# Optimization experiments

Measured on AMD Instinct MI355X. Metric: run time of the kernel, lower is better.

The kernel has to match this reference:

```python
import jax, jax.numpy as jnp
import numpy as np

H = 8        # n_heads (== n_kv_heads)
D = 128      # head_dim
WINDOW = 16  # sliding window (left); causal => right window = 0
EPS = 1e-6   # qk_norm_eps


def rms_norm(x, w, eps=EPS):
    # RMSNorm over last dim with learnable scale
    ms = jnp.mean(jnp.square(x), axis=-1, keepdims=True)
    return x * jax.lax.rsqrt(ms + eps) * w


def setup_inputs() -> dict:
    key = jax.random.key(0)
    ks = jax.random.split(key, 5)
    B, S, dim = 4, 2048, 1024
    scale = 1.0 / np.sqrt(dim)
    return {
        "x": jax.random.normal(ks[0], (B, S, dim), jnp.float32),
        "wq": jax.random.normal(ks[1], (dim, dim), jnp.float32) * scale,
        "wk": jax.random.normal(ks[2], (dim, dim), jnp.float32) * scale,
        "wv": jax.random.normal(ks[3], (dim, dim), jnp.float32) * scale,
        "wo": jax.random.normal(ks[4], (dim, dim), jnp.float32) * scale,
        "q_norm_w": jnp.ones((dim,), jnp.float32),
        "k_norm_w": jnp.ones((dim,), jnp.float32),
    }


def reference(x, wq, wk, wv, wo, q_norm_w, k_norm_w):
    B, S, dim = x.shape
    # projections (torch Linear: x @ W.T)
    xq = rms_norm(x @ wq.T, q_norm_w)
    xk = rms_norm(x @ wk.T, k_norm_w)
    xv = x @ wv.T
    q = xq.reshape(B, S, H, D)
    k = xk.reshape(B, S, H, D)
    v = xv.reshape(B, S, H, D)

    # ALiBi slopes for 8 heads (power of two): 2^-1 .. 2^-8
    slopes = jnp.exp2(-jnp.arange(1, H + 1, dtype=jnp.float32))
    pos = jnp.arange(S)
    rel = pos[None, :] - pos[:, None]          # [S, S], rel[i, j] = j - i
    bias = slopes[:, None, None] * rel.astype(x.dtype)   # [H, S, S]
    masked = (rel > 0) | (rel < -WINDOW)       # causal + sliding window
    bias = jnp.where(masked[None], -jnp.inf, bias)

    scores = jnp.einsum('bqhd,bkhd->bhqk', q, k) / np.sqrt(D) + bias[None]
    attn = jax.nn.softmax(scores, axis=-1)
    out = jnp.einsum('bhqk,bkhd->bqhd', attn, v).reshape(B, S, H * D)
    return out @ wo.T
```

## Files before the change

### kernel.cpp

```cpp
#include <hip/hip_runtime.h>
#include <math.h>

#define NHEADS 8
#define HDIM   128
#define WIN    16
#define DIM    1024
#define QKVDIM 3072
#define SEQ    2048
#define BATCH  4
#define MROWS  (BATCH * SEQ)
#define RMS_EPS 1e-6f

typedef __bf16 bf16x8 __attribute__((ext_vector_type(8)));
typedef unsigned short u16x8 __attribute__((ext_vector_type(8)));
typedef float  f32x4  __attribute__((ext_vector_type(4)));

__device__ __forceinline__ unsigned short f2b(float f) {
    union { float f; unsigned u; } c; c.f = f;
    return (unsigned short)((c.u + 0x7FFFu + ((c.u >> 16) & 1u)) >> 16);
}
__device__ __forceinline__ float b2f(unsigned short u) {
    union { unsigned u; float f; } c; c.u = ((unsigned)u) << 16; return c.f;
}
__device__ __forceinline__ bf16x8 u2b(u16x8 u) {
    union { u16x8 u; bf16x8 b; } c; c.u = u; return c.b;
}

__device__ __forceinline__ void storec(unsigned short* p, float v) { *p = f2b(v); }
__device__ __forceinline__ void storec(float* p, float v) { *p = v; }

__global__ __launch_bounds__(256) void cast_all(const float* __restrict__ x,
                                                const float* __restrict__ w0,
                                                const float* __restrict__ w1,
                                                const float* __restrict__ w2,
                                                const float* __restrict__ w3,
                                                unsigned short* __restrict__ xb,
                                                unsigned short* __restrict__ wb,
                                                float* __restrict__ sumsq)
{
    const int b = blockIdx.x;
    const int t = threadIdx.x;
    if (b >= 12288) {
        ((float4*)sumsq)[(b - 12288) * 256 + t] = make_float4(0.f, 0.f, 0.f, 0.f);
        return;
    }
    const float* src;
    unsigned short* dst;
    int i;
    if (b < 8192) {
        i = b * 256 + t;
        src = x; dst = xb;
    } else {
        const int bb = b - 8192;
        const int which = bb >> 10;
        i = (bb & 1023) * 256 + t;
        src = which == 0 ? w0 : which == 1 ? w1 : which == 2 ? w2 : w3;
        dst = wb + (size_t)which * DIM * DIM;
    }
    const float4 v = ((const float4*)src)[i];
    ushort4 o;
    o.x = f2b(v.x); o.y = f2b(v.y); o.z = f2b(v.z); o.w = f2b(v.w);
    ((ushort4*)dst)[i] = o;
}

template <typename TC>
__global__ __launch_bounds__(256) void gemm_nt_mfma(const unsigned short* __restrict__ A,
                                                    const unsigned short* __restrict__ B,
                                                    TC* __restrict__ C,
                                                    float* __restrict__ sumsq,
                                                    int M, int N, int K)
{
    __shared__ __align__(16) __bf16 As[128 * 64];
    __shared__ __align__(16) __bf16 Bs[128 * 64];

    const int t    = threadIdx.x;
    const int w    = t >> 6;
    const int lane = t & 63;
    const int wm   = w >> 1;
    const int wn   = w & 1;
    const int bm0  = blockIdx.y * 128;
    const int bn0  = blockIdx.x * 128;

    const int lrow   = lane >> 3;
    const int lchunk = (lane & 7) ^ (lrow & 7);
    const size_t laneoff = (size_t)lrow * K + lchunk * 8;

    const unsigned short* gA = A + (size_t)bm0 * K + laneoff;
    const unsigned short* gB = B + (size_t)bn0 * K + laneoff;

    const int frow = lane & 15;
    const int quad = lane >> 4;
    const int cs0 = ((quad    ) ^ (frow & 7)) * 8;
    const int cs1 = ((quad + 4) ^ (frow & 7)) * 8;

    f32x4 acc[4][4];
    #pragma unroll
    for (int i = 0; i < 4; ++i)
        #pragma unroll
        for (int j = 0; j < 4; ++j)
            #pragma unroll
            for (int e = 0; e < 4; ++e) acc[i][j][e] = 0.f;

    for (int kt = 0; kt < K; kt += 64) {
        __syncthreads();
        #pragma unroll
        for (int s = 0; s < 4; ++s) {
            const int seg = w * 4 + s;
            __builtin_amdgcn_global_load_lds(
                (const __attribute__((address_space(1))) void*)(gA + (size_t)seg * 8 * K + kt),
                (__attribute__((address_space(3))) void*)&As[seg * 512], 16, 0, 0);
            __builtin_amdgcn_global_load_lds(
                (const __attribute__((address_space(1))) void*)(gB + (size_t)seg * 8 * K + kt),
                (__attribute__((address_space(3))) void*)&Bs[seg * 512], 16, 0, 0);
        }
        __syncthreads();

        #pragma unroll
        for (int sub = 0; sub < 2; ++sub) {
            const int cs = sub ? cs1 : cs0;
            bf16x8 af[4], bg[4];
            #pragma unroll
            for (int i = 0; i < 4; ++i) {
                af[i] = *(const bf16x8*)&As[(wm * 64 + i * 16 + frow) * 64 + cs];
                bg[i] = *(const bf16x8*)&Bs[(wn * 64 + i * 16 + frow) * 64 + cs];
            }
            #pragma unroll
            for (int i = 0; i < 4; ++i)
                #pragma unroll
                for (int j = 0; j < 4; ++j)
                    acc[i][j] = __builtin_amdgcn_mfma_f32_16x16x32_bf16(af[i], bg[j], acc[i][j], 0, 0, 0);
        }
    }

    const int m_base = bm0 + wm * 64;
    const int n_base = bn0 + wn * 64;
    const int col    = frow;
    const int rquad  = quad * 4;
    #pragma unroll
    for (int i = 0; i < 4; ++i)
        #pragma unroll
        for (int r = 0; r < 4; ++r) {
            TC* crow = C + (size_t)(m_base + i * 16 + rquad + r) * N + n_base + col;
            #pragma unroll
            for (int j = 0; j < 4; ++j)
                storec(crow + j * 16, acc[i][j][r]);
        }

    if (sumsq != nullptr && bn0 < 2 * DIM) {
        const int which = bn0 >> 10;
        #pragma unroll
        for (int i = 0; i < 4; ++i)
            #pragma unroll
            for (int r = 0; r < 4; ++r) {
                float p = acc[i][0][r] * acc[i][0][r] + acc[i][1][r] * acc[i][1][r]
                        + acc[i][2][r] * acc[i][2][r] + acc[i][3][r] * acc[i][3][r];
                p += __shfl_xor(p, 1, 64);
                p += __shfl_xor(p, 2, 64);
                p += __shfl_xor(p, 4, 64);
                p += __shfl_xor(p, 8, 64);
                if (frow == 0)
                    atomicAdd(&sumsq[(size_t)(m_base + i * 16 + rquad + r) * 2 + which], p);
            }
    }
}

__global__ __launch_bounds__(256) void attn_mfma(const unsigned short* __restrict__ qkv,
                                                 const float* __restrict__ sumsq,
                                                 const float* __restrict__ qw,
                                                 const float* __restrict__ kw,
                                                 unsigned short* __restrict__ o)
{
    __shared__ __align__(16) unsigned short Klds[80 * 136];
    __shared__ __align__(16) unsigned short Vt[128 * 88];
    __shared__ __align__(16) unsigned short Plds[4 * 16 * 40];

    const int t  = threadIdx.x;
    const int qb = blockIdx.x;
    const int h  = blockIdx.y;
    const int r0 = qb * 64;
    const int i0 = r0 & (SEQ - 1);
    const int bb = r0 - i0;

    const unsigned short* kg = qkv + DIM + h * HDIM;
    const unsigned short* vg = qkv + 2 * DIM + h * HDIM;

    #pragma unroll
    for (int it = 0; it < 5; ++it) {
        const int c = it * 256 + t;
        {
            const int lr = c >> 4, c8 = c & 15;
            const int ks = i0 - 16 + lr;
            const int rc = ks < 0 ? 0 : ks;
            const float ksc = rsqrtf(sumsq[(size_t)(bb + rc) * 2 + 1] * (1.0f / DIM) + RMS_EPS);
            const u16x8 kv = *(const u16x8*)(kg + (size_t)(bb + rc) * QKVDIM + c8 * 8);
            u16x8 ko;
            #pragma unroll
            for (int e = 0; e < 8; ++e)
                ko[e] = f2b(b2f(kv[e]) * ksc * kw[h * HDIM + c8 * 8 + e]);
            *(u16x8*)&Klds[lr * 136 + c8 * 8] = ko;
        }
        {
            const int c8 = c / 80, lr = c - c8 * 80;
            const int ks = i0 - 16 + lr;
            const int rc = ks < 0 ? 0 : ks;
            const u16x8 vv = *(const u16x8*)(vg + (size_t)(bb + rc) * QKVDIM + c8 * 8);
            #pragma unroll
            for (int e = 0; e < 8; ++e)
                Vt[(c8 * 8 + e) * 88 + lr] = vv[e];
        }
    }
    __syncthreads();

    const int w    = t >> 6;
    const int lane = t & 63;
    const int frow = lane & 15;
    const int quad = lane >> 4;
    const int fk   = quad * 8;

    f32x4 s0 = {0.f, 0.f, 0.f, 0.f}, s1 = {0.f, 0.f, 0.f, 0.f};
    const unsigned short* qg = qkv + h * HDIM;
    const size_t qrow = (size_t)(r0 + w * 16 + frow) * QKVDIM;
    const float qsc = rsqrtf(sumsq[(size_t)(r0 + w * 16 + frow) * 2] * (1.0f / DIM) + RMS_EPS);
    #pragma unroll
    for (int kt = 0; kt < 4; ++kt) {
        const u16x8 qa = *(const u16x8*)(qg + qrow + kt * 32 + fk);
        u16x8 qn;
        #pragma unroll
        for (int e = 0; e < 8; ++e)
            qn[e] = f2b(b2f(qa[e]) * qsc * qw[h * HDIM + kt * 32 + fk + e]);
        const bf16x8 af = u2b(qn);
        const bf16x8 b0 = *(const bf16x8*)&Klds[(w * 16 + frow) * 136 + kt * 32 + fk];
        const bf16x8 b1 = *(const bf16x8*)&Klds[(w * 16 + 16 + frow) * 136 + kt * 32 + fk];
        s0 = __builtin_amdgcn_mfma_f32_16x16x32_bf16(af, b0, s0, 0, 0, 0);
        s1 = __builtin_amdgcn_mfma_f32_16x16x32_bf16(af, b1, s1, 0, 0, 0);
    }

    const float scl   = 0.088388347648318447f;
    const float slope = exp2f(-(float)(h + 1));
    const bool  lead  = (i0 == 0) && (w == 0);
    const int   col   = frow;
    float inv[4];
    #pragma unroll
    for (int r = 0; r < 4; ++r) {
        const int m = quad * 4 + r;
        float v0 = (col < m || lead) ? -1e30f : s0[r] * scl + slope * (float)(col - 16 - m);
        float v1 = (col > m)         ? -1e30f : s1[r] * scl + slope * (float)(col - m);
        float mx = fmaxf(v0, v1);
        #pragma unroll
        for (int off = 1; off < 16; off <<= 1) mx = fmaxf(mx, __shfl_xor(mx, off, 64));
        const float e0 = __expf(v0 - mx);
        const float e1 = __expf(v1 - mx);
        float sm = e0 + e1;
        #pragma unroll
        for (int off = 1; off < 16; off <<= 1) sm += __shfl_xor(sm, off, 64);
        inv[r] = 1.0f / sm;
        Plds[(w * 16 + m) * 40 + col]      = f2b(e0);
        Plds[(w * 16 + m) * 40 + 16 + col] = f2b(e1);
    }

    const bf16x8 pf = *(const bf16x8*)&Plds[(w * 16 + frow) * 40 + fk];
    f32x4 oa[8];
    #pragma unroll
    for (int nt = 0; nt < 8; ++nt) {
        oa[nt][0] = 0.f; oa[nt][1] = 0.f; oa[nt][2] = 0.f; oa[nt][3] = 0.f;
        const bf16x8 vf = *(const bf16x8*)&Vt[(nt * 16 + frow) * 88 + w * 16 + fk];
        oa[nt] = __builtin_amdgcn_mfma_f32_16x16x32_bf16(pf, vf, oa[nt], 0, 0, 0);
    }

    #pragma unroll
    for (int nt = 0; nt < 8; ++nt)
        #pragma unroll
        for (int r = 0; r < 4; ++r) {
            const int m = quad * 4 + r;
            o[(size_t)(r0 + w * 16 + m) * DIM + h * HDIM + nt * 16 + col] =
                f2b(oa[nt][r] * inv[r]);
        }
}

extern "C" void kernel_launch(void* const* d_in, const int* in_sizes, int n_in,
                              void* d_out, int out_size, void* d_ws, size_t ws_size,
                              hipStream_t stream)
{
    const float* x  = (const float*)d_in[0];
    const float* wq = (const float*)d_in[1];
    const float* wk = (const float*)d_in[2];
    const float* wv = (const float*)d_in[3];
    const float* wo = (const float*)d_in[4];
    const float* qw = (const float*)d_in[5];
    const float* kw = (const float*)d_in[6];
    float* out = (float*)d_out;

    unsigned short* xb   = (unsigned short*)d_ws;
    unsigned short* wb   = xb + (size_t)MROWS * DIM;
    unsigned short* xqkv = wb + (size_t)4 * DIM * DIM;
    unsigned short* ob   = xqkv + (size_t)MROWS * QKVDIM;
    float*          ssq  = (float*)(ob + (size_t)MROWS * DIM);
    unsigned short* wob  = wb + (size_t)3 * DIM * DIM;

    cast_all<<<12304, 256, 0, stream>>>(x, wq, wk, wv, wo, xb, wb, ssq);

    gemm_nt_mfma<unsigned short><<<dim3(QKVDIM / 128, MROWS / 128), 256, 0, stream>>>(
        xb, wb, xqkv, ssq, MROWS, QKVDIM, DIM);

    attn_mfma<<<dim3(MROWS / 64, NHEADS), 256, 0, stream>>>(xqkv, ssq, qw, kw, ob);

    gemm_nt_mfma<float><<<dim3(DIM / 128, MROWS / 128), 256, 0, stream>>>(
        ob, wob, out, nullptr, MROWS, DIM, DIM);
}
```

Before: 222.2 us.

## Replace GEMM with 256x256-tile double-buffered ping-pong MFMA kernel

Rewrites the projection GEMM to use 256x256 block tiles with 512 threads (8 waves, 2x4 wave grid), double-buffered LDS and global_load_lds prefetching interleaved with MFMA clusters separated by explicit barriers and vmcnt waits. s_setprio raises priority around MFMA bursts. The aim is to hide global-load latency and raise arithmetic intensity per LDS byte. In exchange it uses 128KB of LDS per block and many more accumulator registers. The larger tiles also give fewer blocks (e.g. 128 for the output GEMM), which may underfill the 256 CUs.

```diff
diff --git a/kernel.cpp b/kernel.cpp
--- a/kernel.cpp
+++ b/kernel.cpp
@@ -63,103 +63,150 @@
     ((ushort4*)dst)[i] = o;
 }
 
+#define BARR do { asm volatile("s_barrier" ::: "memory"); __builtin_amdgcn_sched_barrier(0); } while (0)
+#define WAITV(N) asm volatile("s_waitcnt vmcnt(" #N ")" ::: "memory")
+
+#define LDA8(mh, b) { \
+    _Pragma("unroll") for (int il = 0; il < 4; ++il) { \
+        const int rr = (wm * 128 + (mh) * 64 + il * 16 + frow) * 64; \
+        af[il][0] = *(const bf16x8*)&As[b][rr + cs0]; \
+        af[il][1] = *(const bf16x8*)&As[b][rr + cs1]; \
+    } }
+
+#define LDB4(nh, b, bgr) { \
+    _Pragma("unroll") for (int jl = 0; jl < 2; ++jl) { \
+        const int rr = (wn * 64 + (nh) * 32 + jl * 16 + frow) * 64; \
+        bgr[jl][0] = *(const bf16x8*)&Bs[b][rr + cs0]; \
+        bgr[jl][1] = *(const bf16x8*)&Bs[b][rr + cs1]; \
+    } }
+
+#define MMA16(mh, nh, bgr) { \
+    __builtin_amdgcn_s_setprio(1); \
+    _Pragma("unroll") for (int il = 0; il < 4; ++il) \
+    _Pragma("unroll") for (int jl = 0; jl < 2; ++jl) { \
+        acc[(mh)*4+il][(nh)*2+jl] = __builtin_amdgcn_mfma_f32_16x16x32_bf16(af[il][0], bgr[jl][0], acc[(mh)*4+il][(nh)*2+jl], 0, 0, 0); \
+        acc[(mh)*4+il][(nh)*2+jl] = __builtin_amdgcn_mfma_f32_16x16x32_bf16(af[il][1], bgr[jl][1], acc[(mh)*4+il][(nh)*2+jl], 0, 0, 0); \
+    } \
+    __builtin_amdgcn_s_setprio(0); }
+
+#define STAGE_A(b, half, kt) { \
+    _Pragma("unroll") for (int s2 = 0; s2 < 2; ++s2) { \
+        const int rb = (half) * 128 + s2 * 64; \
+        __builtin_amdgcn_global_load_lds( \
+            (const __attribute__((address_space(1))) void*)(gA + (size_t)rb * K + (kt)), \
+            (__attribute__((address_space(3))) void*)&As[b][(rb + wid * 8) * 64], 16, 0, 0); \
+    } }
+
+#define STAGE_B(b, half, kt) { \
+    _Pragma("unroll") for (int s2 = 0; s2 < 2; ++s2) { \
+        const int rb = (half) * 128 + s2 * 64; \
+        __builtin_amdgcn_global_load_lds( \
+            (const __attribute__((address_space(1))) void*)(gB + (size_t)rb * K + (kt)), \
+            (__attribute__((address_space(3))) void*)&Bs[b][(rb + wid * 8) * 64], 16, 0, 0); \
+    } }
+
 template <typename TC>
-__global__ __launch_bounds__(256) void gemm_nt_mfma(const unsigned short* __restrict__ A,
-                                                    const unsigned short* __restrict__ B,
-                                                    TC* __restrict__ C,
-                                                    float* __restrict__ sumsq,
-                                                    int M, int N, int K)
+__global__ __launch_bounds__(512, 2) void gemm_nt_256(const unsigned short* __restrict__ A,
+                                                      const unsigned short* __restrict__ B,
+                                                      TC* __restrict__ C,
+                                                      float* __restrict__ sumsq,
+                                                      int M, int N, int K)
 {
-    __shared__ __align__(16) __bf16 As[128 * 64];
-    __shared__ __align__(16) __bf16 Bs[128 * 64];
+    __shared__ __align__(16) __bf16 As[2][256 * 64];
+    __shared__ __align__(16) __bf16 Bs[2][256 * 64];
 
     const int t    = threadIdx.x;
-    const int w    = t >> 6;
+    const int wid  = t >> 6;
     const int lane = t & 63;
-    const int wm   = w >> 1;
-    const int wn   = w & 1;
-    const int bm0  = blockIdx.y * 128;
-    const int bn0  = blockIdx.x * 128;
-
-    const int lrow   = lane >> 3;
-    const int lchunk = (lane & 7) ^ (lrow & 7);
-    const size_t laneoff = (size_t)lrow * K + lchunk * 8;
-
-    const unsigned short* gA = A + (size_t)bm0 * K + laneoff;
-    const unsigned short* gB = B + (size_t)bn0 * K + laneoff;
+    const int wm   = wid >> 2;
+    const int wn   = wid & 3;
+    const int bm0  = blockIdx.y * 256;
+    const int bn0  = blockIdx.x * 256;
 
     const int frow = lane & 15;
     const int quad = lane >> 4;
-    const int cs0 = ((quad    ) ^ (frow & 7)) * 8;
-    const int cs1 = ((quad + 4) ^ (frow & 7)) * 8;
-
-    f32x4 acc[4][4];
-    #pragma unroll
-    for (int i = 0; i < 4; ++i)
+    const int cs0  = ((quad    ) ^ (frow & 7)) * 8;
+    const int cs1  = ((quad + 4) ^ (frow & 7)) * 8;
+
+    const int lr = lane >> 3;
+    const int lc = (lane & 7) ^ lr;
+    const unsigned short* gA = A + (size_t)(bm0 + wid * 8 + lr) * K + lc * 8;
+    const unsigned short* gB = B + (size_t)(bn0 + wid * 8 + lr) * K + lc * 8;
+
+    f32x4 acc[8][4];
+    #pragma unroll
+    for (int i = 0; i < 8; ++i)
         #pragma unroll
         for (int j = 0; j < 4; ++j)
             #pragma unroll
             for (int e = 0; e < 4; ++e) acc[i][j][e] = 0.f;
 
-    for (int kt = 0; kt < K; kt += 64) {
-        __syncthreads();
-        #pragma unroll
-        for (int s = 0; s < 4; ++s) {
-            const int seg = w * 4 + s;
-            __builtin_amdgcn_global_load_lds(
-                (const __attribute__((address_space(1))) void*)(gA + (size_t)seg * 8 * K + kt),
-                (__attribute__((address_space(3))) void*)&As[seg * 512], 16, 0, 0);
-            __builtin_amdgcn_global_load_lds(
-                (const __attribute__((address_space(1))) void*)(gB + (size_t)seg * 8 * K + kt),
-                (__attribute__((address_space(3))) void*)&Bs[seg * 512], 16, 0, 0);
-        }
-        __syncthreads();
-
-        #pragma unroll
-        for (int sub = 0; sub < 2; ++sub) {
-            const int cs = sub ? cs1 : cs0;
-            bf16x8 af[4], bg[4];
-            #pragma unroll
-            for (int i = 0; i < 4; ++i) {
-                af[i] = *(const bf16x8*)&As[(wm * 64 + i * 16 + frow) * 64 + cs];
-                bg[i] = *(const bf16x8*)&Bs[(wn * 64 + i * 16 + frow) * 64 + cs];
-            }
-            #pragma unroll
-            for (int i = 0; i < 4; ++i)
-                #pragma unroll
-                for (int j = 0; j < 4; ++j)
-                    acc[i][j] = __builtin_amdgcn_mfma_f32_16x16x32_bf16(af[i], bg[j], acc[i][j], 0, 0, 0);
-        }
-    }
-
-    const int m_base = bm0 + wm * 64;
+    bf16x8 af[4][2], bg0[2][2], bg1[2][2];
+
+    const int NI = K >> 7;
+
+    STAGE_B(0, 0, 0); STAGE_B(0, 1, 0); STAGE_A(0, 0, 0); STAGE_A(0, 1, 0);
+    STAGE_B(1, 0, 64); STAGE_B(1, 1, 64);
+    WAITV(4);
+    BARR;
+
+    for (int i = 0; i < NI; ++i) {
+        const bool last = (i == NI - 1);
+        const int kt0 = i << 7;
+        LDA8(0, 0); LDB4(0, 0, bg0);
+        STAGE_A(1, 0, kt0 + 64);
+        BARR; MMA16(0, 0, bg0); BARR;
+        LDB4(1, 0, bg1);
+        STAGE_A(1, 1, kt0 + 64);
+        BARR; MMA16(0, 1, bg1); BARR;
+        LDA8(1, 0);
+        if (!last) STAGE_B(0, 0, kt0 + 128);
+        BARR; MMA16(1, 1, bg1); BARR;
+        if (!last) STAGE_B(0, 1, kt0 + 128);
+        BARR; MMA16(1, 0, bg0);
+        if (last) { WAITV(0); } else { WAITV(4); }
+        BARR;
+        LDA8(0, 1); LDB4(0, 1, bg0);
+        if (!last) STAGE_A(0, 0, kt0 + 128);
+        BARR; MMA16(0, 0, bg0); BARR;
+        LDB4(1, 1, bg1);
+        if (!last) STAGE_A(0, 1, kt0 + 128);
+        BARR; MMA16(0, 1, bg1); BARR;
+        LDA8(1, 1);
+        if (!last) STAGE_B(1, 0, kt0 + 192);
+        BARR; MMA16(1, 1, bg1); BARR;
+        if (!last) STAGE_B(1, 1, kt0 + 192);
+        BARR; MMA16(1, 0, bg0);
+        if (!last) { WAITV(4); }
+        BARR;
+    }
+
+    const int m_base = bm0 + wm * 128;
     const int n_base = bn0 + wn * 64;
-    const int col    = frow;
-    const int rquad  = quad * 4;
-    #pragma unroll
-    for (int i = 0; i < 4; ++i)
+    #pragma unroll
+    for (int i2 = 0; i2 < 8; ++i2)
         #pragma unroll
         for (int r = 0; r < 4; ++r) {
-            TC* crow = C + (size_t)(m_base + i * 16 + rquad + r) * N + n_base + col;
+            TC* crow = C + (size_t)(m_base + i2 * 16 + quad * 4 + r) * N + n_base + frow;
             #pragma unroll
             for (int j = 0; j < 4; ++j)
-                storec(crow + j * 16, acc[i][j][r]);
+                storec(crow + j * 16, acc[i2][j][r]);
         }
 
     if (sumsq != nullptr && bn0 < 2 * DIM) {
         const int which = bn0 >> 10;
         #pragma unroll
-        for (int i = 0; i < 4; ++i)
+        for (int i2 = 0; i2 < 8; ++i2)
             #pragma unroll
             for (int r = 0; r < 4; ++r) {
-                float p = acc[i][0][r] * acc[i][0][r] + acc[i][1][r] * acc[i][1][r]
-                        + acc[i][2][r] * acc[i][2][r] + acc[i][3][r] * acc[i][3][r];
+                float p = acc[i2][0][r] * acc[i2][0][r] + acc[i2][1][r] * acc[i2][1][r]
+                        + acc[i2][2][r] * acc[i2][2][r] + acc[i2][3][r] * acc[i2][3][r];
                 p += __shfl_xor(p, 1, 64);
                 p += __shfl_xor(p, 2, 64);
                 p += __shfl_xor(p, 4, 64);
                 p += __shfl_xor(p, 8, 64);
                 if (frow == 0)
-                    atomicAdd(&sumsq[(size_t)(m_base + i * 16 + rquad + r) * 2 + which], p);
+                    atomicAdd(&sumsq[(size_t)(m_base + i2 * 16 + quad * 4 + r) * 2 + which], p);
             }
     }
 }
@@ -188,8 +235,8 @@
     for (int it = 0; it < 5; ++it) {
         const int c = it * 256 + t;
         {
-            const int lr = c >> 4, c8 = c & 15;
-            const int ks = i0 - 16 + lr;
+            const int lr2 = c >> 4, c8 = c & 15;
+            const int ks = i0 - 16 + lr2;
             const int rc = ks < 0 ? 0 : ks;
             const float ksc = rsqrtf(sumsq[(size_t)(bb + rc) * 2 + 1] * (1.0f / DIM) + RMS_EPS);
             const u16x8 kv = *(const u16x8*)(kg + (size_t)(bb + rc) * QKVDIM + c8 * 8);
@@ -197,16 +244,16 @@
             #pragma unroll
             for (int e = 0; e < 8; ++e)
                 ko[e] = f2b(b2f(kv[e]) * ksc * kw[h * HDIM + c8 * 8 + e]);
-            *(u16x8*)&Klds[lr * 136 + c8 * 8] = ko;
+            *(u16x8*)&Klds[lr2 * 136 + c8 * 8] = ko;
         }
         {
-            const int c8 = c / 80, lr = c - c8 * 80;
-            const int ks = i0 - 16 + lr;
+            const int c8 = c / 80, lr2 = c - c8 * 80;
+            const int ks = i0 - 16 + lr2;
             const int rc = ks < 0 ? 0 : ks;
             const u16x8 vv = *(const u16x8*)(vg + (size_t)(bb + rc) * QKVDIM + c8 * 8);
             #pragma unroll
             for (int e = 0; e < 8; ++e)
-                Vt[(c8 * 8 + e) * 88 + lr] = vv[e];
+                Vt[(c8 * 8 + e) * 88 + lr2] = vv[e];
         }
     }
     __syncthreads();
@@ -299,11 +346,11 @@
 
     cast_all<<<12304, 256, 0, stream>>>(x, wq, wk, wv, wo, xb, wb, ssq);
 
-    gemm_nt_mfma<unsigned short><<<dim3(QKVDIM / 128, MROWS / 128), 256, 0, stream>>>(
+    gemm_nt_256<unsigned short><<<dim3(QKVDIM / 256, MROWS / 256), 512, 0, stream>>>(
         xb, wb, xqkv, ssq, MROWS, QKVDIM, DIM);
 
     attn_mfma<<<dim3(MROWS / 64, NHEADS), 256, 0, stream>>>(xqkv, ssq, qw, kw, ob);
 
-    gemm_nt_mfma<float><<<dim3(DIM / 128, MROWS / 128), 256, 0, stream>>>(
+    gemm_nt_256<float><<<dim3(DIM / 256, MROWS / 256), 512, 0, stream>>>(
         ob, wob, out, nullptr, MROWS, DIM, DIM);
 }
```

Result: slower. 227.3 us (+2.3%).
